# Kernel tuning notes

Hardware: AMD Instinct MI355X
Metric: run time of the kernel (lower is better)

The kernel has to match this reference:

```python
import jax, jax.numpy as jnp
import numpy as np

FP8_MAX = 448.0  # finfo(float8_e4m3fn).max
EPS = 1e-12
BLK = 128        # weight_block_size = (128, 128); activation group_size = 128


def setup_inputs() -> dict:
    key = jax.random.key(0)
    k1, k2, k3, k4 = jax.random.split(key, 4)
    B, S, H, O = 4, 4096, 2048, 2048
    x = jax.random.normal(k1, (B, S, H), dtype=jnp.float32)
    # fp8 weight: generate, round to e4m3fn grid, store as f32 (values exactly fp8-representable)
    w_raw = jax.random.normal(k2, (O, H), dtype=jnp.float32) * 0.02
    weight = w_raw.astype(jnp.float8_e4m3fn).astype(jnp.float32)
    # per-(128x128)-block weight scales
    weight_scale = jax.random.uniform(k3, (O // BLK, H // BLK), dtype=jnp.float32,
                                      minval=0.001, maxval=0.01)
    bias = jax.random.normal(k4, (O,), dtype=jnp.float32) * 0.01
    return {"x": x, "weight": weight, "weight_scale": weight_scale, "bias": bias}


def reference(x, weight, weight_scale, bias):
    B, S, H = x.shape
    O = weight.shape[0]
    J = H // BLK  # number of activation groups / weight column-blocks
    # per-token-group fp8 quantization (group_size = BLK)
    xg = x.reshape(-1, J, BLK)                                      # [M, J, BLK]
    max_abs = jnp.clip(jnp.max(jnp.abs(xg), axis=-1, keepdims=True), EPS)
    scales = FP8_MAX / max_abs                                      # [M, J, 1]
    xq = jnp.clip(xg * scales, -FP8_MAX, FP8_MAX)
    xq = xq.astype(jnp.float8_e4m3fn).astype(jnp.float32)           # fp8 round-trip
    inv_scale = 1.0 / scales                                        # stored input_scale
    # block-scaled matmul == dequantize both operands then single GEMM
    x_dq = (xq * inv_scale).reshape(-1, H)                          # [M, H]
    w_scale_full = jnp.repeat(jnp.repeat(weight_scale, BLK, axis=0), BLK, axis=1)  # [O, H]
    w_dq = weight * w_scale_full                                    # [O, H]
    y = x_dq @ w_dq.T + bias                                        # [M, O]
    return y.reshape(B, S, O)
```

## Files before the change

### kernel.cpp

```cpp
#include <hip/hip_runtime.h>
#include <cstdint>

#define FP8MAX 448.0f

typedef float f32x4 __attribute__((ext_vector_type(4)));
typedef int   i32x4 __attribute__((ext_vector_type(4)));
typedef int   i32x8 __attribute__((ext_vector_type(8)));

union frag8 { i32x8 v8; i32x4 v4[2]; };

__device__ __forceinline__ void gload_lds16(const void* g, void* l) {
  __builtin_amdgcn_global_load_lds(
      (const __attribute__((address_space(1))) unsigned int*)g,
      (__attribute__((address_space(3))) unsigned int*)l,
      16, 0, 0);
}

__global__ __launch_bounds__(256) void quant_x(const float* __restrict__ x,
                                               uint8_t* __restrict__ xq,
                                               float* __restrict__ sa) {
  const int m = blockIdx.x;
  const int t = threadIdx.x;
  const float* xr = x + (size_t)m * 2048;
  float4 v0 = ((const float4*)xr)[t * 2];
  float4 v1 = ((const float4*)xr)[t * 2 + 1];
  float amax = fmaxf(fmaxf(fmaxf(fabsf(v0.x), fabsf(v0.y)), fmaxf(fabsf(v0.z), fabsf(v0.w))),
                     fmaxf(fmaxf(fabsf(v1.x), fabsf(v1.y)), fmaxf(fabsf(v1.z), fabsf(v1.w))));
  #pragma unroll
  for (int off = 1; off < 16; off <<= 1)
    amax = fmaxf(amax, __shfl_xor(amax, off));
  amax = fmaxf(amax, 1e-12f);
  float s   = FP8MAX / amax;
  float inv = 1.0f / s;
  if ((t & 15) == 0) sa[(size_t)m * 16 + (t >> 4)] = inv;
  float q[8] = {v0.x * s, v0.y * s, v0.z * s, v0.w * s,
                v1.x * s, v1.y * s, v1.z * s, v1.w * s};
  #pragma unroll
  for (int i = 0; i < 8; ++i) q[i] = fminf(fmaxf(q[i], -FP8MAX), FP8MAX);
  union { unsigned long long u; unsigned int w[2]; } pk;
  pk.w[0] = __builtin_amdgcn_cvt_pk_fp8_f32(q[0], q[1], 0, false);
  pk.w[0] = __builtin_amdgcn_cvt_pk_fp8_f32(q[2], q[3], pk.w[0], true);
  pk.w[1] = __builtin_amdgcn_cvt_pk_fp8_f32(q[4], q[5], 0, false);
  pk.w[1] = __builtin_amdgcn_cvt_pk_fp8_f32(q[6], q[7], pk.w[1], true);
  ((unsigned long long*)(xq + (size_t)m * 2048))[t] = pk.u;
}

__global__ __launch_bounds__(256) void conv_w(const float* __restrict__ w,
                                              uint8_t* __restrict__ w8, int n8) {
  int i = blockIdx.x * 256 + threadIdx.x;
  if (i >= n8) return;
  float4 v0 = ((const float4*)w)[i * 2];
  float4 v1 = ((const float4*)w)[i * 2 + 1];
  union { unsigned long long u; unsigned int x[2]; } pk;
  pk.x[0] = __builtin_amdgcn_cvt_pk_fp8_f32(v0.x, v0.y, 0, false);
  pk.x[0] = __builtin_amdgcn_cvt_pk_fp8_f32(v0.z, v0.w, pk.x[0], true);
  pk.x[1] = __builtin_amdgcn_cvt_pk_fp8_f32(v1.x, v1.y, 0, false);
  pk.x[1] = __builtin_amdgcn_cvt_pk_fp8_f32(v1.z, v1.w, pk.x[1], true);
  ((unsigned long long*)w8)[i] = pk.u;
}

__global__ __launch_bounds__(256, 2) void gemm_fp8(
    const uint8_t* __restrict__ A, const uint8_t* __restrict__ Bw,
    const float* __restrict__ sa, const float* __restrict__ sb,
    const float* __restrict__ bias, float* __restrict__ out,
    int M, int N, int K) {
  const int J = K >> 7;
  const int nbn = N >> 7;
  int bid = blockIdx.x;
  int nwg = gridDim.x;
  if ((nwg & 7) == 0) {
    int cpx = nwg >> 3;
    bid = (bid & 7) * cpx + (bid >> 3);
  }
  const int bn = bid % nbn;
  const int bm = bid / nbn;
  const int t = threadIdx.x;
  const int lane = t & 63;
  const int w = t >> 6;
  const int wm = (w >> 1) << 6;
  const int wn = (w & 1) << 6;
  const int r16 = lane & 15;
  const int kg = lane >> 4;

  __shared__ __align__(16) uint8_t lA[2][128 * 128];
  __shared__ __align__(16) uint8_t lB[2][128 * 128];
  __shared__ __align__(16) float sal[16 * 128];

  const uint8_t* gA = A + (size_t)bm * 128 * K;
  const uint8_t* gB = Bw + (size_t)bn * 128 * K;

  for (int i = t; i < 128 * 16; i += 256) {
    int row = i & 127, j = i >> 7;
    sal[j * 128 + row] = sa[((size_t)bm * 128 + row) * 16 + j];
  }

  const int srow = t >> 3;
  const int sg = t & 7;

  #define STAGE(buf_, kt_) do {                                              \
    _Pragma("unroll")                                                        \
    for (int it_ = 0; it_ < 4; ++it_) {                                      \
      int r_ = srow + it_ * 32;                                              \
      int so_ = ((sg ^ (r_ & 7)) << 4);                                      \
      gload_lds16(gA + (size_t)r_ * K + ((kt_) << 7) + so_,                  \
                  &lA[buf_][r_ * 128 + sg * 16]);                            \
      gload_lds16(gB + (size_t)r_ * K + ((kt_) << 7) + so_,                  \
                  &lB[buf_][r_ * 128 + sg * 16]);                            \
    } } while (0)

  __syncthreads();

  STAGE(0, 0);
  STAGE(1, 1);

  f32x4 tot[4][4] = {};
  const f32x4 fz = {0.f, 0.f, 0.f, 0.f};
  frag8 av[4], bv[4];
  f32x4 scq[4];

  int rowA[4], rowB[4];
  #pragma unroll
  for (int a = 0; a < 4; ++a) rowA[a] = wm + a * 16 + r16;
  #pragma unroll
  for (int b = 0; b < 4; ++b) rowB[b] = wn + b * 16 + r16;

  const int KT = K >> 7;
  for (int kt = 0; kt < KT; ++kt) {
    const int cur = kt & 1;
    asm volatile("s_waitcnt vmcnt(8)" ::: "memory");
    __builtin_amdgcn_s_barrier();
    asm volatile("" ::: "memory");
    #pragma unroll
    for (int a = 0; a < 4; ++a) {
      const int sw = (rowA[a] & 7) << 4;
      const uint8_t* bp = &lA[cur][rowA[a] * 128];
      av[a].v4[0] = *(const i32x4*)(bp + ((kg * 32) ^ sw));
      av[a].v4[1] = *(const i32x4*)(bp + ((kg * 32 + 16) ^ sw));
    }
    #pragma unroll
    for (int b = 0; b < 4; ++b) {
      const int sw = (rowB[b] & 7) << 4;
      const uint8_t* bp = &lB[cur][rowB[b] * 128];
      bv[b].v4[0] = *(const i32x4*)(bp + ((kg * 32) ^ sw));
      bv[b].v4[1] = *(const i32x4*)(bp + ((kg * 32 + 16) ^ sw));
    }
    const float sbj = sb[bn * J + kt];
    #pragma unroll
    for (int a = 0; a < 4; ++a)
      scq[a] = (*(const f32x4*)&sal[kt * 128 + wm + a * 16 + kg * 4]) * sbj;
    __builtin_amdgcn_s_setprio(1);
    #pragma unroll
    for (int a = 0; a < 4; ++a) {
      #pragma unroll
      for (int b = 0; b < 4; ++b) {
        f32x4 p = __builtin_amdgcn_mfma_scale_f32_16x16x128_f8f6f4(
            av[a].v8, bv[b].v8, fz, 0, 0, 0, 0x7f7f7f7f, 0, 0x7f7f7f7f);
        tot[a][b] += p * scq[a];
      }
    }
    __builtin_amdgcn_s_setprio(0);
    __builtin_amdgcn_s_barrier();
    asm volatile("" ::: "memory");
    const int kt2 = (kt + 2 < KT) ? kt + 2 : kt + 2 - KT;
    STAGE(cur, kt2);
  }
  asm volatile("s_waitcnt vmcnt(0)" ::: "memory");

  float bb[4];
  #pragma unroll
  for (int b = 0; b < 4; ++b) bb[b] = bias[bn * 128 + wn + b * 16 + r16];
  #pragma unroll
  for (int a = 0; a < 4; ++a) {
    int row0 = bm * 128 + wm + a * 16 + kg * 4;
    #pragma unroll
    for (int r = 0; r < 4; ++r) {
      float* orow = out + (size_t)(row0 + r) * N + bn * 128;
      #pragma unroll
      for (int b = 0; b < 4; ++b)
        orow[wn + b * 16 + r16] = tot[a][b][r] + bb[b];
    }
  }
}

extern "C" void kernel_launch(void* const* d_in, const int* in_sizes, int n_in,
                              void* d_out, int out_size, void* d_ws, size_t ws_size,
                              hipStream_t stream) {
  const float* x    = (const float*)d_in[0];
  const float* wt   = (const float*)d_in[1];
  const float* wsc  = (const float*)d_in[2];
  const float* bias = (const float*)d_in[3];
  float* out = (float*)d_out;

  const int O = in_sizes[3];
  const int H = in_sizes[1] / O;
  const int M = in_sizes[0] / H;

  uint8_t* xq = (uint8_t*)d_ws;
  uint8_t* w8 = xq + (size_t)M * H;
  float*   sa = (float*)(w8 + (size_t)O * H);

  quant_x<<<M, 256, 0, stream>>>(x, xq, sa);
  int n8 = O * H / 8;
  conv_w<<<(n8 + 255) / 256, 256, 0, stream>>>(wt, w8, n8);
  int grid = (M / 128) * (O / 128);
  gemm_fp8<<<grid, 256, 0, stream>>>(xq, w8, sa, wsc, bias, out, M, O, H);
}
```

Before: 147.7 us.

## Pre-swizzle FP8 weights into MFMA fragment order and load B directly from global

The weight conversion kernel now writes FP8 weights in a blocked layout that matches the MFMA B-fragment order, so each lane can fetch its fragment with contiguous 16-byte global loads. The GEMM drops the LDS staging buffer for B and halves LDS use, which may allow more occupancy. The cost is that B fragment loads are issued from global/L2 inside the main loop with no prefetch, so their latency sits directly in front of the MFMAs. The loop also adds an extra barrier, removes setprio, and no longer waits explicitly on vmcnt before reading A from LDS. That last point relies on the compiler's waits for the B loads.

```diff
diff --git a/kernel.cpp b/kernel.cpp
--- a/kernel.cpp
+++ b/kernel.cpp
@@ -46,7 +46,8 @@
 }
 
 __global__ __launch_bounds__(256) void conv_w(const float* __restrict__ w,
-                                              uint8_t* __restrict__ w8, int n8) {
+                                              uint8_t* __restrict__ w8r,
+                                              int n8, int H) {
   int i = blockIdx.x * 256 + threadIdx.x;
   if (i >= n8) return;
   float4 v0 = ((const float4*)w)[i * 2];
@@ -56,11 +57,17 @@
   pk.x[0] = __builtin_amdgcn_cvt_pk_fp8_f32(v0.z, v0.w, pk.x[0], true);
   pk.x[1] = __builtin_amdgcn_cvt_pk_fp8_f32(v1.x, v1.y, 0, false);
   pk.x[1] = __builtin_amdgcn_cvt_pk_fp8_f32(v1.z, v1.w, pk.x[1], true);
-  ((unsigned long long*)w8)[i] = pk.u;
+  const int hb = H >> 3;
+  int o  = i / hb;
+  int kb = (i - o * hb) * 8;
+  const int J = H >> 7;
+  size_t dst = ((((size_t)(o >> 4) * J + (kb >> 7)) * 8 + ((kb >> 4) & 7)) << 8)
+             + ((o & 15) << 4) + (kb & 15);
+  *(unsigned long long*)(w8r + dst) = pk.u;
 }
 
 __global__ __launch_bounds__(256, 2) void gemm_fp8(
-    const uint8_t* __restrict__ A, const uint8_t* __restrict__ Bw,
+    const uint8_t* __restrict__ A, const uint8_t* __restrict__ Br,
     const float* __restrict__ sa, const float* __restrict__ sb,
     const float* __restrict__ bias, float* __restrict__ out,
     int M, int N, int K) {
@@ -83,11 +90,9 @@
   const int kg = lane >> 4;
 
   __shared__ __align__(16) uint8_t lA[2][128 * 128];
-  __shared__ __align__(16) uint8_t lB[2][128 * 128];
   __shared__ __align__(16) float sal[16 * 128];
 
   const uint8_t* gA = A + (size_t)bm * 128 * K;
-  const uint8_t* gB = Bw + (size_t)bn * 128 * K;
 
   for (int i = t; i < 128 * 16; i += 256) {
     int row = i & 127, j = i >> 7;
@@ -97,39 +102,53 @@
   const int srow = t >> 3;
   const int sg = t & 7;
 
-  #define STAGE(buf_, kt_) do {                                              \
+  #define STAGEA(buf_, kt_) do {                                             \
     _Pragma("unroll")                                                        \
-    for (int it_ = 0; it_ < 4; ++it_) {                                      \
+    for (int it_ = 0; it_ < 2; ++it_) {                                      \
       int r_ = srow + it_ * 32;                                              \
       int so_ = ((sg ^ (r_ & 7)) << 4);                                      \
       gload_lds16(gA + (size_t)r_ * K + ((kt_) << 7) + so_,                  \
                   &lA[buf_][r_ * 128 + sg * 16]);                            \
-      gload_lds16(gB + (size_t)r_ * K + ((kt_) << 7) + so_,                  \
-                  &lB[buf_][r_ * 128 + sg * 16]);                            \
+      int r2_ = r_ + 64;                                                     \
+      int so2_ = ((sg ^ (r2_ & 7)) << 4);                                    \
+      gload_lds16(gA + (size_t)r2_ * K + ((kt_) << 7) + so2_,                \
+                  &lA[buf_][r2_ * 128 + sg * 16]);                           \
     } } while (0)
 
   __syncthreads();
 
-  STAGE(0, 0);
-  STAGE(1, 1);
+  STAGEA(0, 0);
+  STAGEA(1, 1);
 
   f32x4 tot[4][4] = {};
   const f32x4 fz = {0.f, 0.f, 0.f, 0.f};
   frag8 av[4], bv[4];
   f32x4 scq[4];
 
-  int rowA[4], rowB[4];
+  int rowA[4];
   #pragma unroll
   for (int a = 0; a < 4; ++a) rowA[a] = wm + a * 16 + r16;
-  #pragma unroll
-  for (int b = 0; b < 4; ++b) rowB[b] = wn + b * 16 + r16;
+
+  const uint8_t* bBase[4];
+  #pragma unroll
+  for (int b = 0; b < 4; ++b) {
+    int ob = bn * 8 + (wn >> 4) + b;
+    bBase[b] = Br + (size_t)ob * J * 2048 + kg * 512 + r16 * 16;
+  }
+
+  asm volatile("s_waitcnt vmcnt(4)" ::: "memory");
+  __builtin_amdgcn_s_barrier();
+  asm volatile("" ::: "memory");
 
   const int KT = K >> 7;
   for (int kt = 0; kt < KT; ++kt) {
     const int cur = kt & 1;
-    asm volatile("s_waitcnt vmcnt(8)" ::: "memory");
-    __builtin_amdgcn_s_barrier();
-    asm volatile("" ::: "memory");
+    #pragma unroll
+    for (int b = 0; b < 4; ++b) {
+      const uint8_t* p = bBase[b] + ((size_t)kt << 11);
+      bv[b].v4[0] = *(const i32x4*)p;
+      bv[b].v4[1] = *(const i32x4*)(p + 256);
+    }
     #pragma unroll
     for (int a = 0; a < 4; ++a) {
       const int sw = (rowA[a] & 7) << 4;
@@ -137,18 +156,10 @@
       av[a].v4[0] = *(const i32x4*)(bp + ((kg * 32) ^ sw));
       av[a].v4[1] = *(const i32x4*)(bp + ((kg * 32 + 16) ^ sw));
     }
-    #pragma unroll
-    for (int b = 0; b < 4; ++b) {
-      const int sw = (rowB[b] & 7) << 4;
-      const uint8_t* bp = &lB[cur][rowB[b] * 128];
-      bv[b].v4[0] = *(const i32x4*)(bp + ((kg * 32) ^ sw));
-      bv[b].v4[1] = *(const i32x4*)(bp + ((kg * 32 + 16) ^ sw));
-    }
     const float sbj = sb[bn * J + kt];
     #pragma unroll
     for (int a = 0; a < 4; ++a)
       scq[a] = (*(const f32x4*)&sal[kt * 128 + wm + a * 16 + kg * 4]) * sbj;
-    __builtin_amdgcn_s_setprio(1);
     #pragma unroll
     for (int a = 0; a < 4; ++a) {
       #pragma unroll
@@ -158,11 +169,12 @@
         tot[a][b] += p * scq[a];
       }
     }
-    __builtin_amdgcn_s_setprio(0);
     __builtin_amdgcn_s_barrier();
     asm volatile("" ::: "memory");
     const int kt2 = (kt + 2 < KT) ? kt + 2 : kt + 2 - KT;
-    STAGE(cur, kt2);
+    STAGEA(cur, kt2);
+    __builtin_amdgcn_s_barrier();
+    asm volatile("" ::: "memory");
   }
   asm volatile("s_waitcnt vmcnt(0)" ::: "memory");
 
@@ -195,13 +207,13 @@
   const int H = in_sizes[1] / O;
   const int M = in_sizes[0] / H;
 
-  uint8_t* xq = (uint8_t*)d_ws;
-  uint8_t* w8 = xq + (size_t)M * H;
-  float*   sa = (float*)(w8 + (size_t)O * H);
+  uint8_t* xq  = (uint8_t*)d_ws;
+  uint8_t* w8r = xq + (size_t)M * H;
+  float*   sa  = (float*)(w8r + (size_t)O * H);
 
   quant_x<<<M, 256, 0, stream>>>(x, xq, sa);
   int n8 = O * H / 8;
-  conv_w<<<(n8 + 255) / 256, 256, 0, stream>>>(wt, w8, n8);
+  conv_w<<<(n8 + 255) / 256, 256, 0, stream>>>(wt, w8r, n8, H);
   int grid = (M / 128) * (O / 128);
-  gemm_fp8<<<grid, 256, 0, stream>>>(xq, w8, sa, wsc, bias, out, M, O, H);
-}
+  gemm_fp8<<<grid, 256, 0, stream>>>(xq, w8r, sa, wsc, bias, out, M, O, H);
+}
```

New measurement: 147.7 us. About the same (+0.0%).
